# Kernel optimization log

Hardware: AMD Instinct MI355X
Metric: run time of the kernel (lower is better)

The kernel has to match this reference:

```python
import jax, jax.numpy as jnp
from jax import lax
import numpy as np

B, CIN, COUT, H, W, K = 32, 128, 256, 64, 64, 3


def _conv_L(x, w, b):
    # pointwise (1x1) conv: x (B,C,H,W), w (Cin,Cout), b (Cout,)
    return jnp.einsum('bchw,co->bohw', x, w) + b[None, :, None, None]


def _dw_along_W(x, w, b):
    # per-channel depthwise 1D correlation along W, VALID padding
    C = x.shape[1]
    y = lax.conv_general_dilated(x, w[:, None, None, :], (1, 1), 'VALID',
                                 dimension_numbers=('NCHW', 'OIHW', 'NCHW'),
                                 feature_group_count=C)
    return y + b[None, :, None, None]


def _dw_along_H(x, w, b):
    # per-channel depthwise 1D correlation along H, VALID padding
    C = x.shape[1]
    y = lax.conv_general_dilated(x, w[:, None, :, None], (1, 1), 'VALID',
                                 dimension_numbers=('NCHW', 'OIHW', 'NCHW'),
                                 feature_group_count=C)
    return y + b[None, :, None, None]


def setup_inputs() -> dict:
    key = jax.random.key(0)
    ks = jax.random.split(key, 13)
    u = lambda kk, shape: jax.random.uniform(kk, shape, jnp.float32, -0.1, 0.1)
    return {
        'x': jax.random.normal(ks[0], (B, CIN, H, W), jnp.float32),
        'L1_w': u(ks[1], (CIN, COUT)), 'L1_b': u(ks[2], (COUT,)),
        'V1_w': u(ks[3], (COUT, K)),   'V1_b': u(ks[4], (COUT,)),
        'H1_w': u(ks[5], (COUT, K)),   'H1_b': u(ks[6], (COUT,)),
        'L2_w': u(ks[7], (COUT, COUT)), 'L2_b': u(ks[8], (COUT,)),
        'V2_w': u(ks[9], (COUT, K)),   'V2_b': u(ks[10], (COUT,)),
        'H2_w': u(ks[11], (COUT, K)),  'H2_b': u(ks[12], (COUT,)),
    }


def reference(x, L1_w, L1_b, V1_w, V1_b, H1_w, H1_b,
              L2_w, L2_b, V2_w, V2_b, H2_w, H2_b):
    p = K // 2
    y = _conv_L(x, L1_w, L1_b)            # (B,COUT,H,W)
    y = _dw_along_H(y, V1_w, V1_b)        # (B,COUT,H-K+1,W)
    y = _dw_along_W(y, H1_w, H1_b)        # (B,COUT,H-K+1,W-K+1)
    y = _conv_L(y, L2_w, L2_b)
    y = jnp.pad(y, ((0, 0), (0, 0), (p, p), (p, p)))  # back to (B,COUT,H,W)
    y = _dw_along_H(y, V2_w, V2_b)
    y = _dw_along_W(y, H2_w, H2_b)        # (B,COUT,H-K+1,W-K+1)
    return y
```

## Files before the change

### kernel.cpp

```cpp
#include <hip/hip_runtime.h>
#include <stdint.h>

#define BB  32
#define CIN 128
#define CO  256
#define HH  64
#define WW  64
#define HW  4096
#define OH  62
#define OW  62
#define OHW 3844

typedef __attribute__((ext_vector_type(8))) short  short8;
typedef __attribute__((ext_vector_type(4))) float  f32x4;
typedef __attribute__((ext_vector_type(4))) ushort ushort4v;
typedef __attribute__((ext_vector_type(2))) ushort ushort2v;
typedef __attribute__((ext_vector_type(2))) float  f32x2;

__device__ __forceinline__ ushort f2bf(float f) {
  uint32_t u = __builtin_bit_cast(uint32_t, f);
  u += 0x7FFFu + ((u >> 16) & 1u);
  return (ushort)(u >> 16);
}
__device__ __forceinline__ float bf2f(ushort h) {
  uint32_t u = ((uint32_t)h) << 16;
  return __builtin_bit_cast(float, u);
}

__global__ void k_wt(const float* __restrict__ w, ushort* __restrict__ wt,
                     int kdim, int ndim) {
  int e = blockIdx.x * 256 + threadIdx.x;
  if (e >= kdim * ndim) return;
  int co = e / kdim, ci = e - co * kdim;
  wt[e] = f2bf(w[(size_t)ci * ndim + co]);
}

template<bool GATHER>
__global__ __launch_bounds__(512) void k_gemm(
    const void* __restrict__ src, const ushort* __restrict__ wt,
    const float* __restrict__ bias, ushort* __restrict__ out,
    int hw_total, int ktot)
{
  __shared__ union alignas(16) {
    struct { ushort Wq[256][40]; ushort Xq[64][40]; } s;
    ushort Cp[256][72];
  } U;
  __shared__ float biasS[256];

  const int t    = threadIdx.x;
  const int b    = blockIdx.y;
  const int hw0  = blockIdx.x * 64;
  const int wid  = t >> 6;
  const int lane = t & 63;
  const int wn   = wid & 3;
  const int wm   = wid >> 2;
  const int l15  = lane & 15;
  const int l4   = lane >> 4;

  if (t < 256) biasS[t] = bias[t];

  f32x4 acc[4][2];
  #pragma unroll
  for (int i = 0; i < 4; ++i)
    #pragma unroll
    for (int j = 0; j < 2; ++j)
      #pragma unroll
      for (int k = 0; k < 4; ++k) acc[i][j][k] = 0.f;

  const int ksteps = ktot >> 5;
  for (int ks = 0; ks < ksteps; ++ks) {
    const int ci0 = ks * 32;
    __syncthreads();

    #pragma unroll
    for (int it = 0; it < 2; ++it) {
      int c  = it * 512 + t;
      int co = c >> 2, seg = c & 3;
      const ushort* p = wt + (size_t)co * ktot + ci0 + seg * 8;
      short8 v = *(const short8*)p;
      *(short8*)&U.s.Wq[co][seg * 8] = v;
    }
    if (t < 256) {
      int hw = t & 63, g = t >> 6;
      short8 v;
      if (GATHER) {
        const float* xp = (const float*)src
            + (size_t)b * CIN * HW + (size_t)(ci0 + g * 8) * HW + hw0 + hw;
        #pragma unroll
        for (int i = 0; i < 8; ++i) v[i] = (short)f2bf(xp[(size_t)i * HW]);
      } else {
        if (hw0 + hw < hw_total) {
          const ushort* xp = (const ushort*)src
              + ((size_t)b * CO + (ci0 + g * 8)) * hw_total + hw0 + hw;
          #pragma unroll
          for (int i = 0; i < 8; ++i) v[i] = (short)xp[(size_t)i * hw_total];
        } else {
          #pragma unroll
          for (int i = 0; i < 8; ++i) v[i] = 0;
        }
      }
      *(short8*)&U.s.Xq[hw][g * 8] = v;
    }
    __syncthreads();

    short8 af[4], bx[2];
    #pragma unroll
    for (int i = 0; i < 4; ++i)
      af[i] = *(const short8*)&U.s.Wq[wn * 64 + i * 16 + l15][l4 * 8];
    #pragma unroll
    for (int j = 0; j < 2; ++j)
      bx[j] = *(const short8*)&U.s.Xq[wm * 32 + j * 16 + l15][l4 * 8];
    #pragma unroll
    for (int i = 0; i < 4; ++i)
      #pragma unroll
      for (int j = 0; j < 2; ++j)
        acc[i][j] = __builtin_amdgcn_mfma_f32_16x16x32_bf16(af[i], bx[j], acc[i][j], 0, 0, 0);
  }

  __syncthreads();

  #pragma unroll
  for (int i = 0; i < 4; ++i) {
    #pragma unroll
    for (int j = 0; j < 2; ++j) {
      int hwl = wm * 32 + j * 16 + l15;
      #pragma unroll
      for (int k = 0; k < 4; ++k) {
        int co = wn * 64 + i * 16 + l4 * 4 + k;
        U.Cp[co][hwl] = f2bf(acc[i][j][k] + biasS[co]);
      }
    }
  }
  __syncthreads();

  const size_t ob = (size_t)b * CO * (size_t)hw_total + hw0;
  if (hw0 + 64 <= hw_total) {
    #pragma unroll
    for (int p = 0; p < 4; ++p) {
      int co = p * 64 + (t >> 3), ch = t & 7;
      ushort4v lo = *(const ushort4v*)&U.Cp[co][ch * 8];
      ushort4v hi = *(const ushort4v*)&U.Cp[co][ch * 8 + 4];
      ushort* q = out + ob + (size_t)co * hw_total + ch * 8;
      *(ushort4v*)q = lo;
      *(ushort4v*)(q + 4) = hi;
    }
  } else {
    int rem = hw_total - hw0;
    #pragma unroll
    for (int p = 0; p < 2; ++p) {
      int co = p * 128 + (t >> 2);
      for (int w = (t & 3); w < rem; w += 4)
        out[ob + (size_t)co * hw_total + w] = U.Cp[co][w];
    }
  }
}

__global__ __launch_bounds__(256) void k_dw1(
    const ushort* __restrict__ y1, const float* __restrict__ vw,
    const float* __restrict__ vb, const float* __restrict__ hwv,
    const float* __restrict__ hb, ushort* __restrict__ t1)
{
  const int t = threadIdx.x, c = blockIdx.x, b = blockIdx.y;
  const int g = t >> 5, l = t & 31;
  const float v0 = vw[c * 3 + 0], v1 = vw[c * 3 + 1], v2 = vw[c * 3 + 2];
  const float q0 = hwv[c * 3 + 0], q1 = hwv[c * 3 + 1], q2 = hwv[c * 3 + 2];
  const float cst = vb[c] * (q0 + q1 + q2) + hb[c];

  const ushort* src = y1 + ((size_t)b * CO + c) * HW;
  ushort*       dst = t1 + ((size_t)b * CO + c) * OHW;
  const int h0s  = g * 8;
  const int hend = (h0s + 7 < OH - 1) ? h0s + 7 : OH - 1;
  const int rend = (h0s + 9 < HH - 1) ? h0s + 9 : HH - 1;
  const int w0 = 2 * l;

  float p0a = 0.f, p0b = 0.f, p1a = 0.f, p1b = 0.f;
  for (int r = h0s; r <= rend; ++r) {
    ushort2v px = *(const ushort2v*)(src + r * WW + w0);
    float xa = bf2f(px[0]), xb = bf2f(px[1]);
    float vva = p0a + v2 * xa, vvb = p0b + v2 * xb;
    p0a = p1a + v1 * xa;  p0b = p1b + v1 * xb;
    p1a = v0 * xa;        p1b = v0 * xb;
    float vvc = __shfl_down(vva, 1, 32);
    float vvd = __shfl_down(vvb, 1, 32);
    int h = r - 2;
    if (h >= h0s && h <= hend && l < 31) {
      ushort2v o;
      o[0] = f2bf(cst + q0 * vva + q1 * vvb + q2 * vvc);
      o[1] = f2bf(cst + q0 * vvb + q1 * vvc + q2 * vvd);
      *(ushort2v*)(dst + h * OW + w0) = o;
    }
  }
}

__global__ __launch_bounds__(256) void k_dw2(
    const ushort* __restrict__ t2, const float* __restrict__ vw,
    const float* __restrict__ vb, const float* __restrict__ hwv,
    const float* __restrict__ hb, float* __restrict__ outp)
{
  const int t = threadIdx.x, c = blockIdx.x, b = blockIdx.y;
  const int g = t >> 5, l = t & 31;
  const float v0 = vw[c * 3 + 0], v1 = vw[c * 3 + 1], v2 = vw[c * 3 + 2];
  const float q0 = hwv[c * 3 + 0], q1 = hwv[c * 3 + 1], q2 = hwv[c * 3 + 2];
  const float cst = vb[c] * (q0 + q1 + q2) + hb[c];

  const ushort* src = t2   + ((size_t)b * CO + c) * OHW;
  float*        dst = outp + ((size_t)b * CO + c) * OHW;
  const int h0s  = g * 8;
  const int hend = (h0s + 7 < OH - 1) ? h0s + 7 : OH - 1;
  const int w0 = 2 * l;

  float p0a = 0.f, p0b = 0.f, p1a = 0.f, p1b = 0.f;
  for (int r = h0s - 1; r <= hend + 1; ++r) {
    float xa = 0.f, xb = 0.f;
    if (r >= 0 && r < OH && l < 31) {
      ushort2v px = *(const ushort2v*)(src + r * OW + w0);
      xa = bf2f(px[0]); xb = bf2f(px[1]);
    }
    float vva = p0a + v2 * xa, vvb = p0b + v2 * xb;
    p0a = p1a + v1 * xa;  p0b = p1b + v1 * xb;
    p1a = v0 * xa;        p1b = v0 * xb;
    float vvL = __shfl_up(vvb, 1, 32);
    float vvR = __shfl_down(vva, 1, 32);
    if (l == 0) vvL = 0.f;
    int h = r - 1;
    if (h >= h0s && h <= hend && l < 31) {
      f32x2 o;
      o[0] = cst + q0 * vvL + q1 * vva + q2 * vvb;
      o[1] = cst + q0 * vva + q1 * vvb + q2 * vvR;
      *(f32x2*)(dst + h * OW + w0) = o;
    }
  }
}

extern "C" void kernel_launch(void* const* d_in, const int* in_sizes, int n_in,
                              void* d_out, int out_size, void* d_ws, size_t ws_size,
                              hipStream_t stream) {
  const float* x   = (const float*)d_in[0];
  const float* L1w = (const float*)d_in[1];
  const float* L1b = (const float*)d_in[2];
  const float* V1w = (const float*)d_in[3];
  const float* V1b = (const float*)d_in[4];
  const float* H1w = (const float*)d_in[5];
  const float* H1b = (const float*)d_in[6];
  const float* L2w = (const float*)d_in[7];
  const float* L2b = (const float*)d_in[8];
  const float* V2w = (const float*)d_in[9];
  const float* V2b = (const float*)d_in[10];
  const float* H2w = (const float*)d_in[11];
  const float* H2b = (const float*)d_in[12];

  char* ws = (char*)d_ws;
  ushort* y1n = (ushort*)ws;
  ushort* w1t = (ushort*)(ws + (size_t)67108864);
  ushort* w2t = (ushort*)(ws + (size_t)67108864 + 65536);
  ushort* t2n = (ushort*)ws;
  ushort* t1n = (ushort*)d_out;

  k_wt<<<dim3((CIN * CO + 255) / 256), dim3(256), 0, stream>>>(L1w, w1t, CIN, CO);
  k_wt<<<dim3((CO * CO + 255) / 256), dim3(256), 0, stream>>>(L2w, w2t, CO, CO);

  k_gemm<true><<<dim3(HW / 64, BB), dim3(512), 0, stream>>>(
      (const void*)x, w1t, L1b, y1n, HW, CIN);

  k_dw1<<<dim3(CO, BB), dim3(256), 0, stream>>>(y1n, V1w, V1b, H1w, H1b, t1n);

  k_gemm<false><<<dim3((OHW + 63) / 64, BB), dim3(512), 0, stream>>>(
      (const void*)t1n, w2t, L2b, t2n, OHW, CO);

  k_dw2<<<dim3(CO, BB), dim3(256), 0, stream>>>(t2n, V2w, V2b, H2w, H2b, (float*)d_out);
}
```

Before: 329.8 us.

## Enlarge GEMM tile, swizzle LDS, store directly, pad intermediate stride

The pointwise GEMM kernel now computes a 128-pixel by 256-channel tile per block, with each wave owning 32 output channels across all 128 pixels. Shared-memory tiles use an XOR swizzle instead of row padding. The epilogue writes bf16 results straight from registers, dropping the LDS staging pass and its extra barriers. The intermediate buffers use a padded per-channel stride of 3968 so the second GEMM needs no bounds checks. The risks are narrower, less coalesced 32-byte global stores per row, and wasted work on the padded columns, which hold uninitialised data.

```diff
diff --git a/kernel.cpp b/kernel.cpp
--- a/kernel.cpp
+++ b/kernel.cpp
@@ -10,12 +10,13 @@
 #define OH  62
 #define OW  62
 #define OHW 3844
+#define OPST 3968
 
 typedef __attribute__((ext_vector_type(8))) short  short8;
 typedef __attribute__((ext_vector_type(4))) float  f32x4;
-typedef __attribute__((ext_vector_type(4))) ushort ushort4v;
 typedef __attribute__((ext_vector_type(2))) ushort ushort2v;
 typedef __attribute__((ext_vector_type(2))) float  f32x2;
+typedef __attribute__((ext_vector_type(2))) uint32_t uint2v;
 
 __device__ __forceinline__ ushort f2bf(float f) {
   uint32_t u = __builtin_bit_cast(uint32_t, f);
@@ -26,6 +27,7 @@
   uint32_t u = ((uint32_t)h) << 16;
   return __builtin_bit_cast(float, u);
 }
+__device__ __forceinline__ int swz16(int C) { return (C ^ ((C >> 2) & 7)) << 4; }
 
 __global__ void k_wt(const float* __restrict__ w, ushort* __restrict__ wt,
                      int kdim, int ndim) {
@@ -36,34 +38,37 @@
 }
 
 template<bool GATHER>
-__global__ __launch_bounds__(512) void k_gemm(
+__global__ __launch_bounds__(512, 4) void k_gemm(
     const void* __restrict__ src, const ushort* __restrict__ wt,
     const float* __restrict__ bias, ushort* __restrict__ out,
-    int hw_total, int ktot)
+    int pst_src, int pst_out, int ktot)
 {
-  __shared__ union alignas(16) {
-    struct { ushort Wq[256][40]; ushort Xq[64][40]; } s;
-    ushort Cp[256][72];
-  } U;
-  __shared__ float biasS[256];
-
-  const int t    = threadIdx.x;
-  const int b    = blockIdx.y;
-  const int hw0  = blockIdx.x * 64;
-  const int wid  = t >> 6;
-  const int lane = t & 63;
-  const int wn   = wid & 3;
-  const int wm   = wid >> 2;
-  const int l15  = lane & 15;
-  const int l4   = lane >> 4;
-
-  if (t < 256) biasS[t] = bias[t];
-
-  f32x4 acc[4][2];
+  __shared__ ushort Wq[256 * 32];
+  __shared__ ushort Xq[128 * 32];
+
+  const int t = threadIdx.x;
+  const int b = blockIdx.y;
+  const int hw0 = blockIdx.x * 128;
+  const int w = t >> 6, lane = t & 63, l15 = lane & 15, l4 = lane >> 4;
+
+  int afoff0, afoff1, bxoff[8], wstoff0, wstoff1, xstoff;
+  afoff0 = swz16((w * 32 + l15) * 4 + l4);
+  afoff1 = swz16((w * 32 + 16 + l15) * 4 + l4);
   #pragma unroll
-  for (int i = 0; i < 4; ++i)
+  for (int j = 0; j < 8; ++j) bxoff[j] = swz16((j * 16 + l15) * 4 + l4);
+  wstoff0 = swz16(t);
+  wstoff1 = swz16(512 + t);
+  const int xhw = t & 127, xg = t >> 7;
+  xstoff = swz16(xhw * 4 + xg);
+
+  const float bias0 = bias[w * 32 + l15];
+  const float bias1 = bias[w * 32 + 16 + l15];
+
+  f32x4 acc[2][8];
+  #pragma unroll
+  for (int i = 0; i < 2; ++i)
     #pragma unroll
-    for (int j = 0; j < 2; ++j)
+    for (int j = 0; j < 8; ++j)
       #pragma unroll
       for (int k = 0; k < 4; ++k) acc[i][j][k] = 0.f;
 
@@ -71,86 +76,54 @@
   for (int ks = 0; ks < ksteps; ++ks) {
     const int ci0 = ks * 32;
     __syncthreads();
-
-    #pragma unroll
-    for (int it = 0; it < 2; ++it) {
-      int c  = it * 512 + t;
-      int co = c >> 2, seg = c & 3;
-      const ushort* p = wt + (size_t)co * ktot + ci0 + seg * 8;
-      short8 v = *(const short8*)p;
-      *(short8*)&U.s.Wq[co][seg * 8] = v;
-    }
-    if (t < 256) {
-      int hw = t & 63, g = t >> 6;
-      short8 v;
+    {
+      int c0 = t, co0 = c0 >> 2, s0 = c0 & 3;
+      short8 v0 = *(const short8*)(wt + (size_t)co0 * ktot + ci0 + s0 * 8);
+      *(short8*)((char*)Wq + wstoff0) = v0;
+      int c1 = 512 + t, co1 = c1 >> 2, s1 = c1 & 3;
+      short8 v1 = *(const short8*)(wt + (size_t)co1 * ktot + ci0 + s1 * 8);
+      *(short8*)((char*)Wq + wstoff1) = v1;
+    }
+    {
+      short8 xv;
       if (GATHER) {
         const float* xp = (const float*)src
-            + (size_t)b * CIN * HW + (size_t)(ci0 + g * 8) * HW + hw0 + hw;
+            + ((size_t)b * ktot + ci0 + xg * 8) * pst_src + hw0 + xhw;
         #pragma unroll
-        for (int i = 0; i < 8; ++i) v[i] = (short)f2bf(xp[(size_t)i * HW]);
+        for (int ii = 0; ii < 8; ++ii) xv[ii] = (short)f2bf(xp[(size_t)ii * pst_src]);
       } else {
-        if (hw0 + hw < hw_total) {
-          const ushort* xp = (const ushort*)src
-              + ((size_t)b * CO + (ci0 + g * 8)) * hw_total + hw0 + hw;
-          #pragma unroll
-          for (int i = 0; i < 8; ++i) v[i] = (short)xp[(size_t)i * hw_total];
-        } else {
-          #pragma unroll
-          for (int i = 0; i < 8; ++i) v[i] = 0;
-        }
+        const ushort* xp = (const ushort*)src
+            + ((size_t)b * ktot + ci0 + xg * 8) * pst_src + hw0 + xhw;
+        #pragma unroll
+        for (int ii = 0; ii < 8; ++ii) xv[ii] = (short)xp[(size_t)ii * pst_src];
       }
-      *(short8*)&U.s.Xq[hw][g * 8] = v;
+      *(short8*)((char*)Xq + xstoff) = xv;
     }
     __syncthreads();
 
-    short8 af[4], bx[2];
+    short8 af0 = *(const short8*)((char*)Wq + afoff0);
+    short8 af1 = *(const short8*)((char*)Wq + afoff1);
     #pragma unroll
-    for (int i = 0; i < 4; ++i)
-      af[i] = *(const short8*)&U.s.Wq[wn * 64 + i * 16 + l15][l4 * 8];
+    for (int j = 0; j < 8; ++j) {
+      short8 bx = *(const short8*)((char*)Xq + bxoff[j]);
+      acc[0][j] = __builtin_amdgcn_mfma_f32_16x16x32_bf16(bx, af0, acc[0][j], 0, 0, 0);
+      acc[1][j] = __builtin_amdgcn_mfma_f32_16x16x32_bf16(bx, af1, acc[1][j], 0, 0, 0);
+    }
+  }
+
+  #pragma unroll
+  for (int i = 0; i < 2; ++i) {
+    const float bi = i ? bias1 : bias0;
+    const int co = w * 32 + i * 16 + l15;
+    ushort* ob = out + (size_t)(b * CO + co) * pst_out + hw0 + l4 * 4;
     #pragma unroll
-    for (int j = 0; j < 2; ++j)
-      bx[j] = *(const short8*)&U.s.Xq[wm * 32 + j * 16 + l15][l4 * 8];
-    #pragma unroll
-    for (int i = 0; i < 4; ++i)
-      #pragma unroll
-      for (int j = 0; j < 2; ++j)
-        acc[i][j] = __builtin_amdgcn_mfma_f32_16x16x32_bf16(af[i], bx[j], acc[i][j], 0, 0, 0);
-  }
-
-  __syncthreads();
-
-  #pragma unroll
-  for (int i = 0; i < 4; ++i) {
-    #pragma unroll
-    for (int j = 0; j < 2; ++j) {
-      int hwl = wm * 32 + j * 16 + l15;
-      #pragma unroll
-      for (int k = 0; k < 4; ++k) {
-        int co = wn * 64 + i * 16 + l4 * 4 + k;
-        U.Cp[co][hwl] = f2bf(acc[i][j][k] + biasS[co]);
-      }
-    }
-  }
-  __syncthreads();
-
-  const size_t ob = (size_t)b * CO * (size_t)hw_total + hw0;
-  if (hw0 + 64 <= hw_total) {
-    #pragma unroll
-    for (int p = 0; p < 4; ++p) {
-      int co = p * 64 + (t >> 3), ch = t & 7;
-      ushort4v lo = *(const ushort4v*)&U.Cp[co][ch * 8];
-      ushort4v hi = *(const ushort4v*)&U.Cp[co][ch * 8 + 4];
-      ushort* q = out + ob + (size_t)co * hw_total + ch * 8;
-      *(ushort4v*)q = lo;
-      *(ushort4v*)(q + 4) = hi;
-    }
-  } else {
-    int rem = hw_total - hw0;
-    #pragma unroll
-    for (int p = 0; p < 2; ++p) {
-      int co = p * 128 + (t >> 2);
-      for (int w = (t & 3); w < rem; w += 4)
-        out[ob + (size_t)co * hw_total + w] = U.Cp[co][w];
+    for (int j = 0; j < 8; ++j) {
+      uint32_t lo = (uint32_t)f2bf(acc[i][j][0] + bi)
+                  | ((uint32_t)f2bf(acc[i][j][1] + bi) << 16);
+      uint32_t hi = (uint32_t)f2bf(acc[i][j][2] + bi)
+                  | ((uint32_t)f2bf(acc[i][j][3] + bi) << 16);
+      uint2v v; v[0] = lo; v[1] = hi;
+      *(uint2v*)(ob + j * 16) = v;
     }
   }
 }
@@ -167,7 +140,7 @@
   const float cst = vb[c] * (q0 + q1 + q2) + hb[c];
 
   const ushort* src = y1 + ((size_t)b * CO + c) * HW;
-  ushort*       dst = t1 + ((size_t)b * CO + c) * OHW;
+  ushort*       dst = t1 + ((size_t)b * CO + c) * OPST;
   const int h0s  = g * 8;
   const int hend = (h0s + 7 < OH - 1) ? h0s + 7 : OH - 1;
   const int rend = (h0s + 9 < HH - 1) ? h0s + 9 : HH - 1;
@@ -203,7 +176,7 @@
   const float q0 = hwv[c * 3 + 0], q1 = hwv[c * 3 + 1], q2 = hwv[c * 3 + 2];
   const float cst = vb[c] * (q0 + q1 + q2) + hb[c];
 
-  const ushort* src = t2   + ((size_t)b * CO + c) * OHW;
+  const ushort* src = t2   + ((size_t)b * CO + c) * OPST;
   float*        dst = outp + ((size_t)b * CO + c) * OHW;
   const int h0s  = g * 8;
   const int hend = (h0s + 7 < OH - 1) ? h0s + 7 : OH - 1;
@@ -259,13 +232,13 @@
   k_wt<<<dim3((CIN * CO + 255) / 256), dim3(256), 0, stream>>>(L1w, w1t, CIN, CO);
   k_wt<<<dim3((CO * CO + 255) / 256), dim3(256), 0, stream>>>(L2w, w2t, CO, CO);
 
-  k_gemm<true><<<dim3(HW / 64, BB), dim3(512), 0, stream>>>(
-      (const void*)x, w1t, L1b, y1n, HW, CIN);
+  k_gemm<true><<<dim3(HW / 128, BB), dim3(512), 0, stream>>>(
+      (const void*)x, w1t, L1b, y1n, HW, HW, CIN);
 
   k_dw1<<<dim3(CO, BB), dim3(256), 0, stream>>>(y1n, V1w, V1b, H1w, H1b, t1n);
 
-  k_gemm<false><<<dim3((OHW + 63) / 64, BB), dim3(512), 0, stream>>>(
-      (const void*)t1n, w2t, L2b, t2n, OHW, CO);
+  k_gemm<false><<<dim3(OPST / 128, BB), dim3(512), 0, stream>>>(
+      (const void*)t1n, w2t, L2b, t2n, OPST, OPST, CO);
 
   k_dw2<<<dim3(CO, BB), dim3(256), 0, stream>>>(t2n, V2w, V2b, H2w, H2b, (float*)d_out);
 }
```

After: 320.2 us. -2.9%, faster.
